# Performance work log

Hardware: AMD Instinct MI355X
Metric: run time of the kernel (lower is better)

The kernel has to match this reference:

```python
import jax, jax.numpy as jnp
import numpy as np

B, L, H, W, C = 2, 32, 16, 16, 32  # L must equal channels for the view() to be consistent
CH = L  # conv channel count


def setup_inputs() -> dict:
    key = jax.random.key(0)
    k1, k2, k3, k4, k5 = jax.random.split(key, 5)
    return {
        "inputs": jax.random.normal(k1, (B, L, H, W, C), dtype=jnp.float32),
        "W1": jax.random.normal(k2, (CH // 2, CH), dtype=jnp.float32) * 0.1,
        "b1": jax.random.normal(k3, (CH // 2,), dtype=jnp.float32) * 0.1,
        "W2": jax.random.normal(k4, (CH, CH), dtype=jnp.float32) * 0.1,
        "b2": jax.random.normal(k5, (CH,), dtype=jnp.float32) * 0.1,
        "gamma": jnp.ones((1,), dtype=jnp.float32),
    }


def reference(inputs, W1, b1, W2, b2, gamma):
    b, l, h, w, c = inputs.shape
    n = l * h * w  # flattened 'spatial' positions after the (buggy-but-faithful) reshape
    # conv1x1 over dim-1 (torch Conv3d treats dim-1 as channels)
    x1 = jnp.einsum('ol,blhwc->bohwc', W1, inputs) + b1[None, :, None, None, None]
    # permute (0,4,1,2,3) then view(b, c//2, l*h*w)
    x1 = jnp.transpose(x1, (0, 4, 1, 2, 3)).reshape(b, c // 2, n)
    # attn[b, i, j] = sum_k x1[b, k, i] * x1[b, k, j]; softmax over last dim
    attn = jax.nn.softmax(jnp.einsum('bki,bkj->bij', x1, x1), axis=-1)  # [b, n, n]
    x2 = jnp.einsum('ol,blhwc->bohwc', W2, inputs) + b2[None, :, None, None, None]
    x2 = jnp.transpose(x2, (0, 4, 1, 2, 3)).reshape(b, c, n)
    # x2 @ attn^T : out[b, c, i] = sum_j x2[b, c, j] * attn[b, i, j]
    out = jnp.einsum('bcj,bij->bci', x2, attn)
    out = jnp.transpose(out.reshape(b, c, l, h, w), (0, 2, 3, 4, 1))
    return out * gamma + inputs
```

## Files before the change

### kernel.cpp

```cpp
#include <hip/hip_runtime.h>
#include <hip/hip_bf16.h>
#include <math.h>

typedef __bf16 bf16x8 __attribute__((ext_vector_type(8)));
typedef __bf16 bf16x2 __attribute__((ext_vector_type(2)));
typedef short  s16x2  __attribute__((ext_vector_type(2)));
typedef short  s16x4  __attribute__((ext_vector_type(4)));
typedef float  floatx16 __attribute__((ext_vector_type(16)));

#define KQ_ELEMS (2 * 8192 * 16)
#define OACC_OFF 1572864
#define SQRT_LOG2E 1.2011224087864498f
#define LSPLIT 4

__global__ __launch_bounds__(256) void proj_kernel(
    const float* __restrict__ in, const float* __restrict__ W1,
    const float* __restrict__ b1, const float* __restrict__ W2,
    const float* __restrict__ b2,
    __hip_bfloat16* __restrict__ Kq, __hip_bfloat16* __restrict__ Vswz,
    float* __restrict__ acc0)
{
    __shared__ float Xs[32][32];
    __shared__ float W1s[16 * 32];
    __shared__ float W2s[32 * 32];
    const int t = threadIdx.x;
    const int bid = blockIdx.x;
    const int b = bid >> 8;
    const int hw = bid & 255;

    {
        int gid = bid * 256 + t;
        *(float4*)(acc0 + (size_t)gid * 4) = make_float4(0.f, 0.f, 0.f, 0.f);
        if (gid < 4096)
            *(float4*)(acc0 + 524288 + (size_t)gid * 4) = make_float4(0.f, 0.f, 0.f, 0.f);
    }

    {
        int l = t >> 3, cs = (t & 7) * 4;
        float4 v = *(const float4*)(in + (((size_t)b * 32 + l) * 256 + hw) * 32 + cs);
        *(float4*)&Xs[l][cs] = v;
    }
    if (t < 128) *(float4*)&W1s[t * 4] = *(const float4*)(W1 + t * 4);
    *(float4*)&W2s[t * 4] = *(const float4*)(W2 + t * 4);
    __syncthreads();

    const int c = t & 31;
    const int g = t >> 5;

#pragma unroll
    for (int oo = 0; oo < 2; ++oo) {
        int o = g * 2 + oo;
        float acc = b1[o];
#pragma unroll
        for (int l = 0; l < 32; ++l) acc += W1s[o * 32 + l] * Xs[l][c];
        int k = c >> 1;
        int i = (c & 1) * 4096 + o * 256 + hw;
        Kq[((size_t)b * 8192 + i) * 16 + k] = __float2bfloat16(acc * SQRT_LOG2E);
    }
#pragma unroll
    for (int oo = 0; oo < 4; ++oo) {
        int o = g * 4 + oo;
        float acc = b2[o];
#pragma unroll
        for (int l = 0; l < 32; ++l) acc += W2s[o * 32 + l] * Xs[l][c];
        int j = o * 256 + hw;
        int jt = j >> 5, rem = j & 31;
        int gg = rem >> 3, h = (rem >> 2) & 1, idx = rem & 3;
        Vswz[(size_t)b * 262144 + jt * 1024 + gg * 256 + h * 128 + c * 4 + idx] =
            __float2bfloat16(acc);
    }
}

__global__ __launch_bounds__(256) void flash_kernel(
    const __hip_bfloat16* __restrict__ Kq, const __hip_bfloat16* __restrict__ Vswz,
    float* __restrict__ Oacc, float* __restrict__ Lacc)
{
    const int t = threadIdx.x;
    const int lane = t & 63;
    const int wv = t >> 6;
    const int m = lane & 31;
    const int h = lane >> 5;

    const int bid = blockIdx.x;
    const int s = bid & ((1 << LSPLIT) - 1);
    const int itile = (bid >> LSPLIT) & 63;
    const int b = bid >> (LSPLIT + 6);
    const int i0 = itile * 128 + wv * 32;
    const int niter = (8192 >> LSPLIT) >> 5;
    const int jt0 = s * niter;

    const __hip_bfloat16* Kb = Kq + (size_t)b * 8192 * 16;
    const __hip_bfloat16* Vb = Vswz + (size_t)b * 262144 + h * 128 + m * 4;

    const bf16x8 bq = *(const bf16x8*)(Kb + (size_t)(i0 + m) * 16 + h * 8);

    floatx16 oa = {}, ob = {};
    float2 l01 = {0.f, 0.f}, l23 = {0.f, 0.f};

#pragma unroll 4
    for (int it = 0; it < niter; ++it) {
        const int jt = jt0 + it;
        bf16x8 ak = *(const bf16x8*)(Kb + (size_t)(jt * 32 + m) * 16 + h * 8);
        s16x4 vf0 = *(const s16x4*)(Vb + (size_t)jt * 1024 + 0);
        s16x4 vf1 = *(const s16x4*)(Vb + (size_t)jt * 1024 + 256);
        s16x4 vf2 = *(const s16x4*)(Vb + (size_t)jt * 1024 + 512);
        s16x4 vf3 = *(const s16x4*)(Vb + (size_t)jt * 1024 + 768);

        floatx16 sc = __builtin_amdgcn_mfma_f32_32x32x16_bf16(ak, bq, (floatx16){}, 0, 0, 0);

#pragma unroll
        for (int g = 0; g < 4; ++g) {
            float e0 = __builtin_amdgcn_exp2f(sc[4 * g + 0]);
            float e1 = __builtin_amdgcn_exp2f(sc[4 * g + 1]);
            float e2 = __builtin_amdgcn_exp2f(sc[4 * g + 2]);
            float e3 = __builtin_amdgcn_exp2f(sc[4 * g + 3]);
            l01.x += e0; l01.y += e1; l23.x += e2; l23.y += e3;
#if defined(__has_builtin) && __has_builtin(__builtin_amdgcn_cvt_pk_bf16_f32)
            bf16x2 plo = __builtin_amdgcn_cvt_pk_bf16_f32(e0, e1);
            bf16x2 phi = __builtin_amdgcn_cvt_pk_bf16_f32(e2, e3);
#else
            bf16x2 plo = {(__bf16)e0, (__bf16)e1};
            bf16x2 phi = {(__bf16)e2, (__bf16)e3};
#endif
            s16x2 lo = __builtin_bit_cast(s16x2, plo);
            s16x2 hi = __builtin_bit_cast(s16x2, phi);
            s16x4 pb = {lo[0], lo[1], hi[0], hi[1]};
            s16x4 vf = (g == 0) ? vf0 : (g == 1) ? vf1 : (g == 2) ? vf2 : vf3;
            if (g < 2)
                oa = __builtin_amdgcn_mfma_f32_32x32x8bf16_1k(pb, vf, oa, 0, 0, 0);
            else
                ob = __builtin_amdgcn_mfma_f32_32x32x8bf16_1k(pb, vf, ob, 0, 0, 0);
        }
    }

    oa = oa + ob;
    float l = (l01.x + l01.y) + (l23.x + l23.y);
    l += __shfl_xor(l, 32);

#pragma unroll
    for (int r = 0; r < 16; ++r) {
        int iloc = (r & 3) + 8 * (r >> 2) + 4 * h;
        size_t row = (size_t)b * 8192 + i0 + iloc;
        unsafeAtomicAdd(&Oacc[row * 32 + m], oa[r]);
    }
    if (h == 0)
        unsafeAtomicAdd(&Lacc[(size_t)b * 8192 + i0 + m], l);
}

__global__ __launch_bounds__(256) void finalize_kernel(
    const float* __restrict__ Oacc, const float* __restrict__ Lacc,
    const float* __restrict__ in, const float* __restrict__ gamma,
    float* __restrict__ out)
{
    const int gid = blockIdx.x * 256 + threadIdx.x;
    const int row = gid >> 3;
    const int c4 = (gid & 7) * 4;
    const size_t base = (size_t)row * 32 + c4;
    float4 o = *(const float4*)(Oacc + base);
    float4 x = *(const float4*)(in + base);
    const float linv = gamma[0] / Lacc[row];
    float4 r;
    r.x = o.x * linv + x.x;
    r.y = o.y * linv + x.y;
    r.z = o.z * linv + x.z;
    r.w = o.w * linv + x.w;
    *(float4*)(out + base) = r;
}

extern "C" void kernel_launch(void* const* d_in, const int* in_sizes, int n_in,
                              void* d_out, int out_size, void* d_ws, size_t ws_size,
                              hipStream_t stream) {
    const float* in = (const float*)d_in[0];
    const float* W1 = (const float*)d_in[1];
    const float* b1 = (const float*)d_in[2];
    const float* W2 = (const float*)d_in[3];
    const float* b2 = (const float*)d_in[4];
    const float* gamma = (const float*)d_in[5];
    float* out = (float*)d_out;

    __hip_bfloat16* Kq = (__hip_bfloat16*)d_ws;
    __hip_bfloat16* Vswz = Kq + KQ_ELEMS;
    float* Oacc = (float*)((char*)d_ws + OACC_OFF);
    float* Lacc = Oacc + 16384 * 32;

    proj_kernel<<<512, 256, 0, stream>>>(in, W1, b1, W2, b2, Kq, Vswz, Oacc);
    flash_kernel<<<2 * 64 * (1 << LSPLIT), 256, 0, stream>>>(Kq, Vswz, Oacc, Lacc);
    finalize_kernel<<<512, 256, 0, stream>>>(Oacc, Lacc, in, gamma, out);
}
```

Before: 113.0 us.

## Replace atomic split-K accumulation with per-split partial buffers and combine pass

```diff
diff --git a/kernel.cpp b/kernel.cpp
--- a/kernel.cpp
+++ b/kernel.cpp
@@ -9,7 +9,7 @@
 typedef float  floatx16 __attribute__((ext_vector_type(16)));
 
 #define KQ_ELEMS (2 * 8192 * 16)
-#define OACC_OFF 1572864
+#define OPART_OFF 1572864
 #define SQRT_LOG2E 1.2011224087864498f
 #define LSPLIT 4
 
@@ -17,8 +17,7 @@
     const float* __restrict__ in, const float* __restrict__ W1,
     const float* __restrict__ b1, const float* __restrict__ W2,
     const float* __restrict__ b2,
-    __hip_bfloat16* __restrict__ Kq, __hip_bfloat16* __restrict__ Vswz,
-    float* __restrict__ acc0)
+    __hip_bfloat16* __restrict__ Kq, __hip_bfloat16* __restrict__ Vswz)
 {
     __shared__ float Xs[32][32];
     __shared__ float W1s[16 * 32];
@@ -27,13 +26,6 @@
     const int bid = blockIdx.x;
     const int b = bid >> 8;
     const int hw = bid & 255;
-
-    {
-        int gid = bid * 256 + t;
-        *(float4*)(acc0 + (size_t)gid * 4) = make_float4(0.f, 0.f, 0.f, 0.f);
-        if (gid < 4096)
-            *(float4*)(acc0 + 524288 + (size_t)gid * 4) = make_float4(0.f, 0.f, 0.f, 0.f);
-    }
 
     {
         int l = t >> 3, cs = (t & 7) * 4;
@@ -73,7 +65,7 @@
 
 __global__ __launch_bounds__(256) void flash_kernel(
     const __hip_bfloat16* __restrict__ Kq, const __hip_bfloat16* __restrict__ Vswz,
-    float* __restrict__ Oacc, float* __restrict__ Lacc)
+    float* __restrict__ Opart, float* __restrict__ Lpart)
 {
     const int t = threadIdx.x;
     const int lane = t & 63;
@@ -141,29 +133,38 @@
     for (int r = 0; r < 16; ++r) {
         int iloc = (r & 3) + 8 * (r >> 2) + 4 * h;
         size_t row = (size_t)b * 8192 + i0 + iloc;
-        unsafeAtomicAdd(&Oacc[row * 32 + m], oa[r]);
+        Opart[((row << LSPLIT) | s) * 32 + m] = oa[r];
     }
     if (h == 0)
-        unsafeAtomicAdd(&Lacc[(size_t)b * 8192 + i0 + m], l);
+        Lpart[(((size_t)b * 8192 + i0 + m) << LSPLIT) | s] = l;
 }
 
-__global__ __launch_bounds__(256) void finalize_kernel(
-    const float* __restrict__ Oacc, const float* __restrict__ Lacc,
+__global__ __launch_bounds__(256) void combine_kernel(
+    const float* __restrict__ Opart, const float* __restrict__ Lpart,
     const float* __restrict__ in, const float* __restrict__ gamma,
     float* __restrict__ out)
 {
     const int gid = blockIdx.x * 256 + threadIdx.x;
     const int row = gid >> 3;
     const int c4 = (gid & 7) * 4;
+    const float* op = Opart + (((size_t)row << LSPLIT)) * 32 + c4;
+    const float* lp = Lpart + ((size_t)row << LSPLIT);
+    float4 acc = make_float4(0.f, 0.f, 0.f, 0.f);
+    float lsum = 0.f;
+#pragma unroll
+    for (int s = 0; s < (1 << LSPLIT); ++s) {
+        float4 v = *(const float4*)(op + s * 32);
+        acc.x += v.x; acc.y += v.y; acc.z += v.z; acc.w += v.w;
+        lsum += lp[s];
+    }
     const size_t base = (size_t)row * 32 + c4;
-    float4 o = *(const float4*)(Oacc + base);
     float4 x = *(const float4*)(in + base);
-    const float linv = gamma[0] / Lacc[row];
+    const float gl = gamma[0] / lsum;
     float4 r;
-    r.x = o.x * linv + x.x;
-    r.y = o.y * linv + x.y;
-    r.z = o.z * linv + x.z;
-    r.w = o.w * linv + x.w;
+    r.x = acc.x * gl + x.x;
+    r.y = acc.y * gl + x.y;
+    r.z = acc.z * gl + x.z;
+    r.w = acc.w * gl + x.w;
     *(float4*)(out + base) = r;
 }
 
@@ -180,10 +181,10 @@
 
     __hip_bfloat16* Kq = (__hip_bfloat16*)d_ws;
     __hip_bfloat16* Vswz = Kq + KQ_ELEMS;
-    float* Oacc = (float*)((char*)d_ws + OACC_OFF);
-    float* Lacc = Oacc + 16384 * 32;
+    float* Opart = (float*)((char*)d_ws + OPART_OFF);
+    float* Lpart = Opart + ((size_t)16384 << LSPLIT) * 32;
 
-    proj_kernel<<<512, 256, 0, stream>>>(in, W1, b1, W2, b2, Kq, Vswz, Oacc);
-    flash_kernel<<<2 * 64 * (1 << LSPLIT), 256, 0, stream>>>(Kq, Vswz, Oacc, Lacc);
-    finalize_kernel<<<512, 256, 0, stream>>>(Oacc, Lacc, in, gamma, out);
+    proj_kernel<<<512, 256, 0, stream>>>(in, W1, b1, W2, b2, Kq, Vswz);
+    flash_kernel<<<2 * 64 * (1 << LSPLIT), 256, 0, stream>>>(Kq, Vswz, Opart, Lpart);
+    combine_kernel<<<512, 256, 0, stream>>>(Opart, Lpart, in, gamma, out);
 }
```

After: 114.1 us. About the same (+0.9%).
